# Kernel optimization log

Measured on AMD Instinct MI355X. Metric: run time of the kernel, lower is better.

## Reference

```python
import jax, jax.numpy as jnp
import numpy as np
from jax import lax

NUM_CLASSES = 10
NUM_ITER = 3
DN = ('NCHW', 'OIHW', 'NCHW')


def squash(t, axis=-1):
    sq = (t ** 2).sum(axis=axis, keepdims=True)
    return (sq / (1.0 + sq)) * t / jnp.sqrt(sq)


def setup_inputs() -> dict:
    key = jax.random.key(0)
    ks = jax.random.split(key, 12)
    B = 512
    s = 0.05  # param scale for numerical stability
    return {
        'x': jax.random.normal(ks[0], (B, 1, 28, 28), jnp.float32),
        'conv1_w': jax.random.normal(ks[1], (256, 1, 9, 9), jnp.float32) * s,
        'conv1_b': jax.random.normal(ks[2], (256,), jnp.float32) * s,
        'prim_w': jax.random.normal(ks[3], (8, 32, 256, 9, 9), jnp.float32) * s,
        'prim_b': jax.random.normal(ks[4], (8, 32), jnp.float32) * s,
        'route_w': jax.random.normal(ks[5], (NUM_CLASSES, 32 * 6 * 6, 8, 16), jnp.float32),
        'dec_w1': jax.random.normal(ks[6], (512, 16 * NUM_CLASSES), jnp.float32) * s,
        'dec_b1': jax.random.normal(ks[7], (512,), jnp.float32) * s,
        'dec_w2': jax.random.normal(ks[8], (1024, 512), jnp.float32) * s,
        'dec_b2': jax.random.normal(ks[9], (1024,), jnp.float32) * s,
        'dec_w3': jax.random.normal(ks[10], (784, 1024), jnp.float32) * s,
        'dec_b3': jax.random.normal(ks[11], (784,), jnp.float32) * s,
    }


def reference(x, conv1_w, conv1_b, prim_w, prim_b, route_w,
              dec_w1, dec_b1, dec_w2, dec_b2, dec_w3, dec_b3):
    B = x.shape[0]
    # conv1 + relu: [B,256,20,20]
    h = lax.conv_general_dilated(x, conv1_w, (1, 1), 'VALID', dimension_numbers=DN)
    h = jax.nn.relu(h + conv1_b[None, :, None, None])
    # primary capsules: 8 parallel convs fused into one conv with 8*32 out channels
    kw = prim_w.reshape(8 * 32, 256, 9, 9)
    u = lax.conv_general_dilated(h, kw, (2, 2), 'VALID', dimension_numbers=DN)
    u = u + prim_b.reshape(-1)[None, :, None, None]          # [B,256,6,6]
    u = u.reshape(B, 8, 32 * 6 * 6).transpose(0, 2, 1)       # [B,1152,8]
    u = squash(u, axis=-1)
    # digit capsules: priors [C,B,R,16]
    priors = jnp.einsum('bri,crio->cbro', u, route_w)
    logits = jnp.zeros_like(priors)
    for i in range(NUM_ITER):
        probs = jax.nn.softmax(logits, axis=2)
        v = squash((probs * priors).sum(axis=2, keepdims=True))  # [C,B,1,16]
        if i != NUM_ITER - 1:
            logits = logits + (priors * v).sum(axis=-1, keepdims=True)
    caps = v.squeeze(2).transpose(1, 0, 2)                    # [B,C,16]
    classes = jnp.sqrt((caps ** 2).sum(axis=-1))              # [B,C]
    classes = jax.nn.softmax(classes, axis=1)
    y = jax.nn.one_hot(jnp.argmax(classes, axis=1), NUM_CLASSES, dtype=caps.dtype)
    d = (caps * y[:, :, None]).reshape(B, -1)                 # [B,160]
    d = jax.nn.relu(d @ dec_w1.T + dec_b1)
    d = jax.nn.relu(d @ dec_w2.T + dec_b2)
    recon = jax.nn.sigmoid(d @ dec_w3.T + dec_b3)             # [B,784]
    return classes, recon
```

## Files before the change

### kernel.cpp

```cpp
#include <hip/hip_runtime.h>
#include <math.h>


typedef _Float16 f16;
typedef _Float16 f16x8 __attribute__((ext_vector_type(8)));
typedef _Float16 f16x4 __attribute__((ext_vector_type(4)));
typedef float f32x4 __attribute__((ext_vector_type(4)));

__device__ __forceinline__ void gl_lds16(const void* g, void* l) {
  __builtin_amdgcn_global_load_lds(
      (const __attribute__((address_space(1))) void*)g,
      (__attribute__((address_space(3))) void*)l, 16, 0, 0);
}

__global__ __launch_bounds__(256, 2) void conv1_kernel(
    const float* __restrict__ x, const float* __restrict__ w,
    const float* __restrict__ bias, f16* __restrict__ ht)
{
  __shared__ float xs[364];
  const int b = blockIdx.x;
  const int y0 = blockIdx.y * 5;
  const int t = threadIdx.x;
  for (int i = t; i < 364; i += 256) xs[i] = x[b * 784 + y0 * 28 + i];
  float wr[81];
#pragma unroll
  for (int k = 0; k < 81; ++k) wr[k] = w[t * 81 + k];
  const float bv = bias[t];
  __syncthreads();
  for (int oy = y0; oy < y0 + 5; ++oy) {
    float acc[20];
#pragma unroll
    for (int i = 0; i < 20; ++i) acc[i] = bv;
#pragma unroll
    for (int ky = 0; ky < 9; ++ky) {
      float xr[28];
#pragma unroll
      for (int q = 0; q < 7; ++q) {
        const float4 v = *(const float4*)&xs[(oy - y0 + ky) * 28 + q * 4];
        xr[q*4+0] = v.x; xr[q*4+1] = v.y; xr[q*4+2] = v.z; xr[q*4+3] = v.w;
      }
#pragma unroll
      for (int kx = 0; kx < 9; ++kx) {
        const float wv = wr[ky * 9 + kx];
#pragma unroll
        for (int ox = 0; ox < 20; ++ox) acc[ox] = fmaf(xr[ox + kx], wv, acc[ox]);
      }
    }
    f16* hp = &ht[(size_t)((b * 20 + oy) * 20) * 256 + t];
#pragma unroll
    for (int ox = 0; ox < 20; ++ox)
      hp[ox * 256] = (f16)fmaxf(acc[ox], 0.f);
  }
}

__global__ __launch_bounds__(256) void wtrans_kernel(
    const float* __restrict__ w, f16* __restrict__ wt)
{
  __shared__ float tile[64 * 83];
  const int oc = blockIdx.x;
  const int icq = blockIdx.y;
  const int t = threadIdx.x;
  const float* src = w + (size_t)oc * 20736 + (size_t)icq * 64 * 81;
  for (int idx = t; idx < 5184; idx += 256) {
    const int ici = idx / 81, kk = idx - ici * 81;
    tile[ici * 83 + kk] = src[idx];
  }
  __syncthreads();
  f16* dst = wt + (size_t)oc * 20736 + icq * 64;
  for (int idx = t; idx < 5184; idx += 256) {
    const int kk = idx >> 6, ici = idx & 63;
    dst[kk * 256 + ici] = (f16)tile[ici * 83 + kk];
  }
}

__global__ __launch_bounds__(256) void prim_mfma_kernel(
    const f16* __restrict__ ht, const f16* __restrict__ wt,
    float* __restrict__ part)
{
  __shared__ f16 sm[16384];
  const int t = threadIdx.x;
  const int wv = t >> 6, lane = t & 63;
  const int id = blockIdx.x;
  const int g = id >> 3;
  const int ks = g & 3;
  const int nb = (g >> 2) & 1;
  const int mb = (id & 7) + 8 * (g >> 3);
  const int m0 = mb * 128, n0 = nb * 128;

  const int chunk = (lane & 3) ^ ((lane >> 3) & 3);
  long aoff[2], boff[2];
#pragma unroll
  for (int i = 0; i < 2; ++i) {
    const int r = wv * 32 + i * 16 + (lane >> 2);
    const int m = m0 + r;
    const int b = m / 36, pos = m - b * 36;
    const int oy = pos / 6, ox = pos - oy * 6;
    aoff[i] = (long)(((b * 20 + 2 * oy) * 20 + 2 * ox) * 256) * 2 + chunk * 16;
    boff[i] = (long)(n0 + r) * 41472 + chunk * 16;
  }
  const char* htc = (const char*)ht;
  const char* wtc = (const char*)wt;

  const int lrow = lane & 15, quad = lane >> 4;
  const int qx = quad ^ ((lrow >> 1) & 3);
  const int wm = wv & 1, wn = wv >> 1;
  f32x4 acc[4][4] = {};

  const int s0 = ks * 162, s1 = s0 + 162;

#define STAGE(S, BUFB)                                                        \
  {                                                                           \
    const int kykx = (S) >> 3, icb = (S) & 7;                                 \
    const int ky = kykx / 9, kx = kykx - ky * 9;                              \
    const long astep = (long)((((ky * 20 + kx) * 256) + icb * 32) * 2);       \
    const long bstep = (long)(((kykx * 256) + icb * 32) * 2);                 \
    char* dA = (char*)sm + (BUFB) + wv * 2048;                                \
    char* dB = (char*)sm + (BUFB) + 8192 + wv * 2048;                         \
    gl_lds16(htc + aoff[0] + astep, dA);                                      \
    gl_lds16(htc + aoff[1] + astep, dA + 1024);                               \
    gl_lds16(wtc + boff[0] + bstep, dB);                                      \
    gl_lds16(wtc + boff[1] + bstep, dB + 1024);                               \
  }

#define CONSUME(BUFI)                                                         \
  {                                                                           \
    const f16* As = sm + (BUFI);                                              \
    const f16* Bs = sm + (BUFI) + 4096;                                       \
    f16x8 af[4], bf[4];                                                       \
    _Pragma("unroll") for (int mt = 0; mt < 4; ++mt)                          \
        af[mt] = *(const f16x8*)&As[(wm * 64 + mt * 16 + lrow) * 32 + qx * 8];\
    _Pragma("unroll") for (int nt = 0; nt < 4; ++nt)                          \
        bf[nt] = *(const f16x8*)&Bs[(wn * 64 + nt * 16 + lrow) * 32 + qx * 8];\
    _Pragma("unroll") for (int mt = 0; mt < 4; ++mt)                          \
        _Pragma("unroll") for (int nt = 0; nt < 4; ++nt)                      \
            acc[mt][nt] = __builtin_amdgcn_mfma_f32_16x16x32_f16(             \
                af[mt], bf[nt], acc[mt][nt], 0, 0, 0);                        \
  }

  STAGE(s0, 0);
  for (int s = s0; s < s1; s += 2) {
    __syncthreads();
    STAGE(s + 1, 16384);
    CONSUME(0);
    __syncthreads();
    if (s + 2 < s1) STAGE(s + 2, 0);
    CONSUME(8192);
  }
#undef STAGE
#undef CONSUME

  float* pp = part + (size_t)ks * 4718592;
#pragma unroll
  for (int mt = 0; mt < 4; ++mt) {
    const int mbase = m0 + wm * 64 + mt * 16 + quad * 4;
#pragma unroll
    for (int nt = 0; nt < 4; ++nt) {
      const int n = n0 + wn * 64 + nt * 16 + lrow;
      const int np = (n & 31) * 8 + (n >> 5);
#pragma unroll
      for (int rg = 0; rg < 4; ++rg)
        pp[(size_t)(mbase + rg) * 256 + np] = acc[mt][nt][rg];
    }
  }
}

__global__ void squash_kernel(const float* __restrict__ part,
                              const float* __restrict__ bias,
                              float* __restrict__ u)
{
  const int tid = blockIdx.x * 256 + threadIdx.x;
  if (tid >= 512 * 36 * 32) return;
  const int cc = tid & 31;
  const int row = tid >> 5;
  const int b = row / 36;
  const int pos = row - b * 36;
  const float* p = part + (size_t)row * 256 + cc * 8;
  float v[8] = {};
#pragma unroll
  for (int ksl = 0; ksl < 4; ++ksl) {
    const float4 a0 = *(const float4*)(p + (size_t)ksl * 4718592);
    const float4 a1 = *(const float4*)(p + (size_t)ksl * 4718592 + 4);
    v[0] += a0.x; v[1] += a0.y; v[2] += a0.z; v[3] += a0.w;
    v[4] += a1.x; v[5] += a1.y; v[6] += a1.z; v[7] += a1.w;
  }
  float sq = 0.f;
#pragma unroll
  for (int i = 0; i < 8; ++i) {
    v[i] += bias[i * 32 + cc];
    sq = fmaf(v[i], v[i], sq);
  }
  const float scale = sq / ((1.f + sq) * sqrtf(sq));
  float* up = &u[(size_t)(b * 1152 + cc * 36 + pos) * 8];
#pragma unroll
  for (int i = 0; i < 8; ++i) up[i] = v[i] * scale;
}

__global__ __launch_bounds__(256, 4) void priors_kernel(
    const float* __restrict__ u, const float* __restrict__ rw,
    f16* __restrict__ P)
{
  const int t = threadIdx.x;
  const int rl = t >> 2, oq = t & 3;
  const int r = blockIdx.x * 64 + rl;
  const int b0 = blockIdx.y * 64;
  const int c = blockIdx.z;

  float4 wreg[8];
  const float* wbase = rw + (size_t)(c * 1152 + r) * 128 + oq * 4;
#pragma unroll
  for (int k = 0; k < 8; ++k)
    wreg[k] = *(const float4*)(wbase + k * 16);

  f16* pbase = P + (size_t)((c * 512 + b0) * 1152 + r) * 16 + oq * 4;
  const float* ubase = u + (size_t)(b0 * 1152 + r) * 8;

  for (int b = 0; b < 64; ++b) {
    const float4 ua = *(const float4*)(ubase + (size_t)b * 9216);
    const float4 ub = *(const float4*)(ubase + (size_t)b * 9216 + 4);
    const float uu[8] = {ua.x, ua.y, ua.z, ua.w, ub.x, ub.y, ub.z, ub.w};
    float ax = 0.f, ay = 0.f, az = 0.f, aw = 0.f;
#pragma unroll
    for (int k = 0; k < 8; ++k) {
      ax = fmaf(uu[k], wreg[k].x, ax);
      ay = fmaf(uu[k], wreg[k].y, ay);
      az = fmaf(uu[k], wreg[k].z, az);
      aw = fmaf(uu[k], wreg[k].w, aw);
    }
    f16x4 st;
    st[0] = (f16)ax; st[1] = (f16)ay; st[2] = (f16)az; st[3] = (f16)aw;
    *(f16x4*)(pbase + (size_t)b * 18432) = st;
  }
}

__device__ __forceinline__ float wave_sum(float v) {
#pragma unroll
  for (int off = 32; off > 0; off >>= 1) v += __shfl_xor(v, off);
  return v;
}
__device__ __forceinline__ float wave_max(float v) {
#pragma unroll
  for (int off = 32; off > 0; off >>= 1) v = fmaxf(v, __shfl_xor(v, off));
  return v;
}

__global__ __launch_bounds__(256, 2) void routing_kernel(
    const f16* __restrict__ Pg, float* __restrict__ caps)
{
  const int c = blockIdx.x >> 9;
  const int b = blockIdx.x & 511;
  const int t = threadIdx.x;
  const int wid = t >> 6;
  const int lane = t & 63;
  __shared__ float xred[4 * 17];

  float P[5][16];
  float lg[5];
  const int nk = (t < 128) ? 5 : 4;
#pragma unroll
  for (int k = 0; k < 5; ++k)
#pragma unroll
    for (int o = 0; o < 16; ++o) P[k][o] = 0.f;

  const f16* pbase = Pg + (size_t)((c * 512 + b) * 1152) * 16;
#pragma unroll
  for (int k = 0; k < 5; ++k) {
    if (k < nk) {
      const int r = t + (k << 8);
      const f16x8 p0 = *(const f16x8*)&pbase[(size_t)r * 16];
      const f16x8 p1 = *(const f16x8*)&pbase[(size_t)r * 16 + 8];
#pragma unroll
      for (int o = 0; o < 8; ++o) {
        P[k][o]     = (float)p0[o];
        P[k][o + 8] = (float)p1[o];
      }
    }
  }

  float v[16];
  {
    float sq = 0.f;
#pragma unroll
    for (int o = 0; o < 16; ++o) {
      float p = 0.f;
#pragma unroll
      for (int k = 0; k < 5; ++k) p += P[k][o];
      p = wave_sum(p);
      if (lane == 0) xred[wid * 17 + o] = p;
      v[o] = 0.f;
    }
    __syncthreads();
#pragma unroll
    for (int o = 0; o < 16; ++o) {
      const float s = (xred[o] + xred[17 + o] + xred[34 + o] + xred[51 + o]) *
                      (1.f / 1152.f);
      v[o] = s;
      sq = fmaf(s, s, sq);
    }
    const float scale = sq / ((1.f + sq) * sqrtf(sq));
#pragma unroll
    for (int o = 0; o < 16; ++o) v[o] *= scale;
    __syncthreads();
  }
#pragma unroll
  for (int k = 0; k < 5; ++k) {
    float a = 0.f;
#pragma unroll
    for (int o = 0; o < 16; ++o) a = fmaf(P[k][o], v[o], a);
    lg[k] = a;
  }

  for (int it = 1; it < 3; ++it) {
    float m = -1e30f;
#pragma unroll
    for (int k = 0; k < 5; ++k) if (k < nk) m = fmaxf(m, lg[k]);
    m = wave_max(m);
    if (lane == 0) xred[wid * 17 + 16] = m;
    __syncthreads();
    const float mx = fmaxf(fmaxf(xred[16], xred[17 + 16]),
                           fmaxf(xred[34 + 16], xred[51 + 16]));
    __syncthreads();
    float e[5];
#pragma unroll
    for (int k = 0; k < 5; ++k) e[k] = (k < nk) ? expf(lg[k] - mx) : 0.f;
    float pS = 0.f;
#pragma unroll
    for (int k = 0; k < 5; ++k) pS += e[k];
    pS = wave_sum(pS);
    if (lane == 0) xred[wid * 17 + 16] = pS;
#pragma unroll
    for (int o = 0; o < 16; ++o) {
      float p = 0.f;
#pragma unroll
      for (int k = 0; k < 5; ++k) p = fmaf(e[k], P[k][o], p);
      p = wave_sum(p);
      if (lane == 0) xred[wid * 17 + o] = p;
    }
    __syncthreads();
    const float S = xred[16] + xred[17 + 16] + xred[34 + 16] + xred[51 + 16];
    const float inv = 1.f / S;
    float sq = 0.f;
#pragma unroll
    for (int o = 0; o < 16; ++o) {
      const float s = (xred[o] + xred[17 + o] + xred[34 + o] + xred[51 + o]) * inv;
      v[o] = s;
      sq = fmaf(s, s, sq);
    }
    const float scale = sq / ((1.f + sq) * sqrtf(sq));
#pragma unroll
    for (int o = 0; o < 16; ++o) v[o] *= scale;
    __syncthreads();
    if (it < 2) {
#pragma unroll
      for (int k = 0; k < 5; ++k) {
        float a = 0.f;
#pragma unroll
        for (int o = 0; o < 16; ++o) a = fmaf(P[k][o], v[o], a);
        lg[k] += a;
      }
    }
  }
  if (t == 0) {
    float* cp = &caps[(b * 10 + c) * 16];
#pragma unroll
    for (int o = 0; o < 16; ++o) cp[o] = v[o];
  }
}

__global__ void classes_kernel(const float* __restrict__ caps,
                               float* __restrict__ out_classes,
                               float* __restrict__ d0)
{
  const int b = blockIdx.x * 256 + threadIdx.x;
  if (b >= 512) return;
  float nrm[10];
#pragma unroll
  for (int cc = 0; cc < 10; ++cc) {
    float sq = 0.f;
#pragma unroll
    for (int o = 0; o < 16; ++o) {
      const float vv = caps[(b * 10 + cc) * 16 + o];
      sq = fmaf(vv, vv, sq);
    }
    nrm[cc] = sqrtf(sq);
  }
  float mx = nrm[0]; int cs = 0;
#pragma unroll
  for (int cc = 1; cc < 10; ++cc)
    if (nrm[cc] > mx) { mx = nrm[cc]; cs = cc; }
  float e[10], ssum = 0.f;
#pragma unroll
  for (int cc = 0; cc < 10; ++cc) { e[cc] = expf(nrm[cc] - mx); ssum += e[cc]; }
  const float inv = 1.f / ssum;
#pragma unroll
  for (int cc = 0; cc < 10; ++cc) out_classes[b * 10 + cc] = e[cc] * inv;
#pragma unroll
  for (int cc = 0; cc < 10; ++cc)
#pragma unroll
    for (int o = 0; o < 16; ++o)
      d0[b * 160 + cc * 16 + o] = (cc == cs) ? caps[(b * 10 + cc) * 16 + o] : 0.f;
}

__global__ __launch_bounds__(256, 2) void fc_kernel(
    const float* __restrict__ A, const float* __restrict__ W,
    const float* __restrict__ bias, float* __restrict__ C,
    int N, int K, int act)
{
  __shared__ float As[64][17];
  __shared__ float Ws[64][17];
  const int t = threadIdx.x;
  const int tm = t >> 4, tn = t & 15;
  const int m0 = blockIdx.y << 6, n0 = blockIdx.x << 6;
  const int lr = t >> 2, lq = (t & 3) << 2;
  float acc[4][4] = {};
  for (int k0 = 0; k0 < K; k0 += 16) {
    const float4 av = *(const float4*)&A[(m0 + lr) * K + k0 + lq];
    float4 wv = make_float4(0.f, 0.f, 0.f, 0.f);
    const int wn = n0 + lr;
    if (wn < N) wv = *(const float4*)&W[wn * K + k0 + lq];
    __syncthreads();
    As[lr][lq+0] = av.x; As[lr][lq+1] = av.y; As[lr][lq+2] = av.z; As[lr][lq+3] = av.w;
    Ws[lr][lq+0] = wv.x; Ws[lr][lq+1] = wv.y; Ws[lr][lq+2] = wv.z; Ws[lr][lq+3] = wv.w;
    __syncthreads();
#pragma unroll
    for (int kk = 0; kk < 16; ++kk) {
      float a[4], w[4];
#pragma unroll
      for (int i = 0; i < 4; ++i) a[i] = As[tm * 4 + i][kk];
#pragma unroll
      for (int j = 0; j < 4; ++j) w[j] = Ws[tn * 4 + j][kk];
#pragma unroll
      for (int i = 0; i < 4; ++i)
#pragma unroll
        for (int j = 0; j < 4; ++j) acc[i][j] = fmaf(a[i], w[j], acc[i][j]);
    }
  }
#pragma unroll
  for (int i = 0; i < 4; ++i) {
    const int m = m0 + tm * 4 + i;
#pragma unroll
    for (int j = 0; j < 4; ++j) {
      const int n = n0 + tn * 4 + j;
      if (n < N) {
        float vv = acc[i][j] + bias[n];
        vv = act ? (1.f / (1.f + expf(-vv))) : fmaxf(vv, 0.f);
        C[m * N + n] = vv;
      }
    }
  }
}

extern "C" void kernel_launch(void* const* d_in, const int* in_sizes, int n_in,
                              void* d_out, int out_size, void* d_ws, size_t ws_size,
                              hipStream_t stream)
{
  const float* x       = (const float*)d_in[0];
  const float* conv1_w = (const float*)d_in[1];
  const float* conv1_b = (const float*)d_in[2];
  const float* prim_w  = (const float*)d_in[3];
  const float* prim_b  = (const float*)d_in[4];
  const float* route_w = (const float*)d_in[5];
  const float* dec_w1  = (const float*)d_in[6];
  const float* dec_b1  = (const float*)d_in[7];
  const float* dec_w2  = (const float*)d_in[8];
  const float* dec_b2  = (const float*)d_in[9];
  const float* dec_w3  = (const float*)d_in[10];
  const float* dec_b3  = (const float*)d_in[11];
  float* out = (float*)d_out;

  char* ws = (char*)d_ws;
  f16*   ht   = (f16*)(ws);
  f16*   wtp  = (f16*)(ws + 104857600);
  float* part = (float*)(ws + 115474432);
  float* u    = (float*)(ws + 190971904);
  f16*   P    = (f16*)(ws);
  float* caps = (float*)(ws + 209846272);
  float* d0   = (float*)(ws + 210173952);
  float* d1   = (float*)(ws + 210501632);
  float* d2   = (float*)(ws + 211550208);

  hipLaunchKernelGGL(conv1_kernel, dim3(512, 4), dim3(256), 0, stream,
                     x, conv1_w, conv1_b, ht);
  hipLaunchKernelGGL(wtrans_kernel, dim3(256, 4), dim3(256), 0, stream,
                     prim_w, wtp);
  hipLaunchKernelGGL(prim_mfma_kernel, dim3(1152), dim3(256), 0, stream,
                     ht, wtp, part);
  hipLaunchKernelGGL(squash_kernel, dim3(2304), dim3(256), 0, stream,
                     part, prim_b, u);
  hipLaunchKernelGGL(priors_kernel, dim3(18, 8, 10), dim3(256), 0, stream,
                     u, route_w, P);
  hipLaunchKernelGGL(routing_kernel, dim3(5120), dim3(256), 0, stream,
                     P, caps);
  hipLaunchKernelGGL(classes_kernel, dim3(2), dim3(256), 0, stream,
                     caps, out, d0);
  hipLaunchKernelGGL(fc_kernel, dim3(8, 8), dim3(256), 0, stream,
                     d0, dec_w1, dec_b1, d1, 512, 160, 0);
  hipLaunchKernelGGL(fc_kernel, dim3(16, 8), dim3(256), 0, stream,
                     d1, dec_w2, dec_b2, d2, 1024, 512, 0);
  hipLaunchKernelGGL(fc_kernel, dim3(13, 8), dim3(256), 0, stream,
                     d2, dec_w3, dec_b3, out + 5120, 784, 1024, 1);
}
```

Baseline: 799.7 us.

## Pre-swizzle primary-capsule weights into MFMA fragment order and load B directly to registers

The weight transpose kernel now writes prim weights in a fragment-ready layout, so each lane can load its 8-element B operand for the MFMA directly from global memory into registers. This removes B staging through LDS and halves the shared-memory footprint, with B fragments double-buffered in registers. It also reorders the squashed capsule layout (pos-major instead of channel-major), with the priors kernel remapping route weight indices to match, which should make the squash stores more contiguous. The risk is that direct global loads of B may expose more latency, and the per-wave B loads are repeated across blocks that share the same weights.

```diff
diff --git a/kernel.cpp b/kernel.cpp
--- a/kernel.cpp
+++ b/kernel.cpp
@@ -54,30 +54,31 @@
 }
 
 __global__ __launch_bounds__(256) void wtrans_kernel(
-    const float* __restrict__ w, f16* __restrict__ wt)
-{
-  __shared__ float tile[64 * 83];
+    const float* __restrict__ w, f16* __restrict__ wtf)
+{
+  __shared__ f16 ls[20736];
   const int oc = blockIdx.x;
-  const int icq = blockIdx.y;
+  const int T = oc >> 4, lrow = oc & 15;
   const int t = threadIdx.x;
-  const float* src = w + (size_t)oc * 20736 + (size_t)icq * 64 * 81;
-  for (int idx = t; idx < 5184; idx += 256) {
-    const int ici = idx / 81, kk = idx - ici * 81;
-    tile[ici * 83 + kk] = src[idx];
-  }
+  const float* src = w + (size_t)oc * 20736;
+  for (int idx = t; idx < 20736; idx += 256) ls[idx] = (f16)src[idx];
   __syncthreads();
-  f16* dst = wt + (size_t)oc * 20736 + icq * 64;
-  for (int idx = t; idx < 5184; idx += 256) {
-    const int kk = idx >> 6, ici = idx & 63;
-    dst[kk * 256 + ici] = (f16)tile[ici * 83 + kk];
+  for (int c = t; c < 2592; c += 256) {
+    const int s = c >> 2, quad = c & 3;
+    const int kykx = s >> 3, icb = s & 7;
+    f16x8 v;
+#pragma unroll
+    for (int j = 0; j < 8; ++j)
+      v[j] = ls[(icb * 32 + quad * 8 + j) * 81 + kykx];
+    *(f16x8*)&wtf[((size_t)(T * 648 + s) * 64 + quad * 16 + lrow) * 8] = v;
   }
 }
 
 __global__ __launch_bounds__(256) void prim_mfma_kernel(
-    const f16* __restrict__ ht, const f16* __restrict__ wt,
+    const f16* __restrict__ ht, const f16* __restrict__ wtf,
     float* __restrict__ part)
 {
-  __shared__ f16 sm[16384];
+  __shared__ f16 smA[8192];
   const int t = threadIdx.x;
   const int wv = t >> 6, lane = t & 63;
   const int id = blockIdx.x;
@@ -88,7 +89,7 @@
   const int m0 = mb * 128, n0 = nb * 128;
 
   const int chunk = (lane & 3) ^ ((lane >> 3) & 3);
-  long aoff[2], boff[2];
+  long aoff[2];
 #pragma unroll
   for (int i = 0; i < 2; ++i) {
     const int r = wv * 32 + i * 16 + (lane >> 2);
@@ -96,57 +97,65 @@
     const int b = m / 36, pos = m - b * 36;
     const int oy = pos / 6, ox = pos - oy * 6;
     aoff[i] = (long)(((b * 20 + 2 * oy) * 20 + 2 * ox) * 256) * 2 + chunk * 16;
-    boff[i] = (long)(n0 + r) * 41472 + chunk * 16;
   }
   const char* htc = (const char*)ht;
-  const char* wtc = (const char*)wt;
 
   const int lrow = lane & 15, quad = lane >> 4;
   const int qx = quad ^ ((lrow >> 1) & 3);
   const int wm = wv & 1, wn = wv >> 1;
+
+  const f16* bp[4];
+#pragma unroll
+  for (int nt = 0; nt < 4; ++nt)
+    bp[nt] = wtf + (size_t)(nb * 8 + wn * 4 + nt) * 648 * 512 + lane * 8;
+
   f32x4 acc[4][4] = {};
-
   const int s0 = ks * 162, s1 = s0 + 162;
 
-#define STAGE(S, BUFB)                                                        \
+#define STAGE_A(S, BUFB)                                                      \
   {                                                                           \
     const int kykx = (S) >> 3, icb = (S) & 7;                                 \
     const int ky = kykx / 9, kx = kykx - ky * 9;                              \
     const long astep = (long)((((ky * 20 + kx) * 256) + icb * 32) * 2);       \
-    const long bstep = (long)(((kykx * 256) + icb * 32) * 2);                 \
-    char* dA = (char*)sm + (BUFB) + wv * 2048;                                \
-    char* dB = (char*)sm + (BUFB) + 8192 + wv * 2048;                         \
+    char* dA = (char*)smA + (BUFB) + wv * 2048;                               \
     gl_lds16(htc + aoff[0] + astep, dA);                                      \
     gl_lds16(htc + aoff[1] + astep, dA + 1024);                               \
-    gl_lds16(wtc + boff[0] + bstep, dB);                                      \
-    gl_lds16(wtc + boff[1] + bstep, dB + 1024);                               \
-  }
-
-#define CONSUME(BUFI)                                                         \
+  }
+
+#define CONSUME(BUFI, BF)                                                     \
   {                                                                           \
-    const f16* As = sm + (BUFI);                                              \
-    const f16* Bs = sm + (BUFI) + 4096;                                       \
-    f16x8 af[4], bf[4];                                                       \
+    const f16* As = smA + (BUFI);                                             \
+    f16x8 af[4];                                                              \
     _Pragma("unroll") for (int mt = 0; mt < 4; ++mt)                          \
         af[mt] = *(const f16x8*)&As[(wm * 64 + mt * 16 + lrow) * 32 + qx * 8];\
-    _Pragma("unroll") for (int nt = 0; nt < 4; ++nt)                          \
-        bf[nt] = *(const f16x8*)&Bs[(wn * 64 + nt * 16 + lrow) * 32 + qx * 8];\
     _Pragma("unroll") for (int mt = 0; mt < 4; ++mt)                          \
         _Pragma("unroll") for (int nt = 0; nt < 4; ++nt)                      \
             acc[mt][nt] = __builtin_amdgcn_mfma_f32_16x16x32_f16(             \
-                af[mt], bf[nt], acc[mt][nt], 0, 0, 0);                        \
-  }
-
-  STAGE(s0, 0);
+                af[mt], (BF)[nt], acc[mt][nt], 0, 0, 0);                      \
+  }
+
+  f16x8 bfA[4], bfB[4];
+#pragma unroll
+  for (int nt = 0; nt < 4; ++nt)
+    bfA[nt] = *(const f16x8*)(bp[nt] + (size_t)s0 * 512);
+  STAGE_A(s0, 0);
   for (int s = s0; s < s1; s += 2) {
     __syncthreads();
-    STAGE(s + 1, 16384);
-    CONSUME(0);
-    __syncthreads();
-    if (s + 2 < s1) STAGE(s + 2, 0);
-    CONSUME(8192);
-  }
-#undef STAGE
+    STAGE_A(s + 1, 8192);
+#pragma unroll
+    for (int nt = 0; nt < 4; ++nt)
+      bfB[nt] = *(const f16x8*)(bp[nt] + (size_t)(s + 1) * 512);
+    CONSUME(0, bfA);
+    __syncthreads();
+    if (s + 2 < s1) {
+      STAGE_A(s + 2, 0);
+#pragma unroll
+      for (int nt = 0; nt < 4; ++nt)
+        bfA[nt] = *(const f16x8*)(bp[nt] + (size_t)(s + 2) * 512);
+    }
+    CONSUME(4096, bfB);
+  }
+#undef STAGE_A
 #undef CONSUME
 
   float* pp = part + (size_t)ks * 4718592;
@@ -190,7 +199,7 @@
     sq = fmaf(v[i], v[i], sq);
   }
   const float scale = sq / ((1.f + sq) * sqrtf(sq));
-  float* up = &u[(size_t)(b * 1152 + cc * 36 + pos) * 8];
+  float* up = &u[(size_t)(b * 1152 + pos * 32 + cc) * 8];
 #pragma unroll
   for (int i = 0; i < 8; ++i) up[i] = v[i] * scale;
 }
@@ -201,18 +210,20 @@
 {
   const int t = threadIdx.x;
   const int rl = t >> 2, oq = t & 3;
-  const int r = blockIdx.x * 64 + rl;
+  const int rs = blockIdx.x * 64 + rl;
+  const int pos = rs >> 5, cc = rs & 31;
+  const int r_true = cc * 36 + pos;
   const int b0 = blockIdx.y * 64;
   const int c = blockIdx.z;
 
   float4 wreg[8];
-  const float* wbase = rw + (size_t)(c * 1152 + r) * 128 + oq * 4;
+  const float* wbase = rw + (size_t)(c * 1152 + r_true) * 128 + oq * 4;
 #pragma unroll
   for (int k = 0; k < 8; ++k)
     wreg[k] = *(const float4*)(wbase + k * 16);
 
-  f16* pbase = P + (size_t)((c * 512 + b0) * 1152 + r) * 16 + oq * 4;
-  const float* ubase = u + (size_t)(b0 * 1152 + r) * 8;
+  f16* pbase = P + (size_t)((c * 512 + b0) * 1152 + rs) * 16 + oq * 4;
+  const float* ubase = u + (size_t)(b0 * 1152 + rs) * 8;
 
   for (int b = 0; b < 64; ++b) {
     const float4 ua = *(const float4*)(ubase + (size_t)b * 9216);
@@ -469,7 +480,7 @@
 
   char* ws = (char*)d_ws;
   f16*   ht   = (f16*)(ws);
-  f16*   wtp  = (f16*)(ws + 104857600);
+  f16*   wtf  = (f16*)(ws + 104857600);
   float* part = (float*)(ws + 115474432);
   float* u    = (float*)(ws + 190971904);
   f16*   P    = (f16*)(ws);
@@ -480,10 +491,10 @@
 
   hipLaunchKernelGGL(conv1_kernel, dim3(512, 4), dim3(256), 0, stream,
                      x, conv1_w, conv1_b, ht);
-  hipLaunchKernelGGL(wtrans_kernel, dim3(256, 4), dim3(256), 0, stream,
-                     prim_w, wtp);
+  hipLaunchKernelGGL(wtrans_kernel, dim3(256), dim3(256), 0, stream,
+                     prim_w, wtf);
   hipLaunchKernelGGL(prim_mfma_kernel, dim3(1152), dim3(256), 0, stream,
-                     ht, wtp, part);
+                     ht, wtf, part);
   hipLaunchKernelGGL(squash_kernel, dim3(2304), dim3(256), 0, stream,
                      part, prim_b, u);
   hipLaunchKernelGGL(priors_kernel, dim3(18, 8, 10), dim3(256), 0, stream,
```

Measured after the change: 820.4 us. +2.6%, slower.

## Run conv1 as im2col plus MFMA GEMM and store squashed capsules in fp16

Applied to the files above, without the earlier changes.

Replaces the direct FP32 conv1 with an im2col pass into a padded fp16 matrix (K=96), a transposed fp16 weight, and a 128x128-tile MFMA GEMM with fused bias and ReLU. Squash now writes fp16 capsules in a position-major order, and priors reads them with a single vector load while remapping route weights to the true capsule index. This moves conv1 FLOPs onto matrix cores and halves capsule traffic. In exchange it adds two extra kernels, the im2col buffer traffic, and fp16 rounding of the conv1 inputs and weights.

```diff
diff --git a/kernel.cpp b/kernel.cpp
--- a/kernel.cpp
+++ b/kernel.cpp
@@ -13,43 +13,102 @@
       (__attribute__((address_space(3))) void*)l, 16, 0, 0);
 }
 
-__global__ __launch_bounds__(256, 2) void conv1_kernel(
-    const float* __restrict__ x, const float* __restrict__ w,
+__global__ void im2col_kernel(const float* __restrict__ x, f16* __restrict__ A)
+{
+  const int c = blockIdx.x * 256 + threadIdx.x;
+  const int m = c / 12, kc = c - m * 12;
+  const int b = m / 400, rem = m - b * 400;
+  const int oy = rem / 20, ox = rem - oy * 20;
+  const float* xb = x + b * 784;
+  f16x8 v;
+#pragma unroll
+  for (int j = 0; j < 8; ++j) {
+    const int k = kc * 8 + j;
+    float val = 0.f;
+    if (k < 81) {
+      const int ky = k / 9, kx = k - ky * 9;
+      val = xb[(oy + ky) * 28 + ox + kx];
+    }
+    v[j] = (f16)val;
+  }
+  *(f16x8*)&A[(size_t)m * 96 + kc * 8] = v;
+}
+
+__global__ void c1trans_kernel(const float* __restrict__ w, f16* __restrict__ wt1)
+{
+  const int idx = blockIdx.x * 256 + threadIdx.x;
+  const int oc = idx / 96, k = idx - oc * 96;
+  wt1[idx] = (k < 81) ? (f16)w[oc * 81 + k] : (f16)0.f;
+}
+
+__global__ __launch_bounds__(256) void conv1_mfma_kernel(
+    const f16* __restrict__ A, const f16* __restrict__ wt1,
     const float* __restrict__ bias, f16* __restrict__ ht)
 {
-  __shared__ float xs[364];
-  const int b = blockIdx.x;
-  const int y0 = blockIdx.y * 5;
+  __shared__ f16 sm[8192];
   const int t = threadIdx.x;
-  for (int i = t; i < 364; i += 256) xs[i] = x[b * 784 + y0 * 28 + i];
-  float wr[81];
-#pragma unroll
-  for (int k = 0; k < 81; ++k) wr[k] = w[t * 81 + k];
-  const float bv = bias[t];
-  __syncthreads();
-  for (int oy = y0; oy < y0 + 5; ++oy) {
-    float acc[20];
-#pragma unroll
-    for (int i = 0; i < 20; ++i) acc[i] = bv;
-#pragma unroll
-    for (int ky = 0; ky < 9; ++ky) {
-      float xr[28];
-#pragma unroll
-      for (int q = 0; q < 7; ++q) {
-        const float4 v = *(const float4*)&xs[(oy - y0 + ky) * 28 + q * 4];
-        xr[q*4+0] = v.x; xr[q*4+1] = v.y; xr[q*4+2] = v.z; xr[q*4+3] = v.w;
-      }
-#pragma unroll
-      for (int kx = 0; kx < 9; ++kx) {
-        const float wv = wr[ky * 9 + kx];
-#pragma unroll
-        for (int ox = 0; ox < 20; ++ox) acc[ox] = fmaf(xr[ox + kx], wv, acc[ox]);
-      }
-    }
-    f16* hp = &ht[(size_t)((b * 20 + oy) * 20) * 256 + t];
-#pragma unroll
-    for (int ox = 0; ox < 20; ++ox)
-      hp[ox * 256] = (f16)fmaxf(acc[ox], 0.f);
+  const int wv = t >> 6, lane = t & 63;
+  const int id = blockIdx.x;
+  const int mb = id >> 1, nb = id & 1;
+  const int m0 = mb * 128, n0 = nb * 128;
+
+  const int chunk = (lane & 3) ^ ((lane >> 3) & 3);
+  long aoff[2], boff[2];
+#pragma unroll
+  for (int i = 0; i < 2; ++i) {
+    const int r = wv * 32 + i * 16 + (lane >> 2);
+    aoff[i] = (long)(m0 + r) * 192 + chunk * 16;
+    boff[i] = (long)(n0 + r) * 192 + chunk * 16;
+  }
+  const char* ac = (const char*)A;
+  const char* bc = (const char*)wt1;
+
+  const int lrow = lane & 15, quad = lane >> 4;
+  const int qx = quad ^ ((lrow >> 1) & 3);
+  const int wm = wv & 1, wn = wv >> 1;
+  f32x4 acc[4][4] = {};
+
+  for (int s = 0; s < 3; ++s) {
+    const long kstep = (long)s * 64;
+    __syncthreads();
+    {
+      char* dA = (char*)sm + wv * 2048;
+      char* dB = (char*)sm + 8192 + wv * 2048;
+      gl_lds16(ac + aoff[0] + kstep, dA);
+      gl_lds16(ac + aoff[1] + kstep, dA + 1024);
+      gl_lds16(bc + boff[0] + kstep, dB);
+      gl_lds16(bc + boff[1] + kstep, dB + 1024);
+    }
+    __syncthreads();
+    const f16* As = sm;
+    const f16* Bs = sm + 4096;
+    f16x8 af[4], bf[4];
+#pragma unroll
+    for (int mt = 0; mt < 4; ++mt)
+      af[mt] = *(const f16x8*)&As[(wm * 64 + mt * 16 + lrow) * 32 + qx * 8];
+#pragma unroll
+    for (int nt = 0; nt < 4; ++nt)
+      bf[nt] = *(const f16x8*)&Bs[(wn * 64 + nt * 16 + lrow) * 32 + qx * 8];
+#pragma unroll
+    for (int mt = 0; mt < 4; ++mt)
+#pragma unroll
+      for (int nt = 0; nt < 4; ++nt)
+        acc[mt][nt] = __builtin_amdgcn_mfma_f32_16x16x32_f16(
+            af[mt], bf[nt], acc[mt][nt], 0, 0, 0);
+  }
+
+#pragma unroll
+  for (int nt = 0; nt < 4; ++nt) {
+    const int n = n0 + wn * 64 + nt * 16 + lrow;
+    const float bv = bias[n];
+#pragma unroll
+    for (int mt = 0; mt < 4; ++mt) {
+      const int mbase = m0 + wm * 64 + mt * 16 + quad * 4;
+#pragma unroll
+      for (int rg = 0; rg < 4; ++rg)
+        ht[(size_t)(mbase + rg) * 256 + n] =
+            (f16)fmaxf(acc[mt][nt][rg] + bv, 0.f);
+    }
   }
 }
 
@@ -166,7 +225,7 @@
 
 __global__ void squash_kernel(const float* __restrict__ part,
                               const float* __restrict__ bias,
-                              float* __restrict__ u)
+                              f16* __restrict__ u16)
 {
   const int tid = blockIdx.x * 256 + threadIdx.x;
   if (tid >= 512 * 36 * 32) return;
@@ -190,41 +249,43 @@
     sq = fmaf(v[i], v[i], sq);
   }
   const float scale = sq / ((1.f + sq) * sqrtf(sq));
-  float* up = &u[(size_t)(b * 1152 + cc * 36 + pos) * 8];
-#pragma unroll
-  for (int i = 0; i < 8; ++i) up[i] = v[i] * scale;
+  f16x8 st;
+#pragma unroll
+  for (int i = 0; i < 8; ++i) st[i] = (f16)(v[i] * scale);
+  *(f16x8*)&u16[(size_t)(b * 1152 + pos * 32 + cc) * 8] = st;
 }
 
 __global__ __launch_bounds__(256, 4) void priors_kernel(
-    const float* __restrict__ u, const float* __restrict__ rw,
+    const f16* __restrict__ u16, const float* __restrict__ rw,
     f16* __restrict__ P)
 {
   const int t = threadIdx.x;
   const int rl = t >> 2, oq = t & 3;
-  const int r = blockIdx.x * 64 + rl;
+  const int rs = blockIdx.x * 64 + rl;
+  const int pos = rs >> 5, cc = rs & 31;
+  const int r_true = cc * 36 + pos;
   const int b0 = blockIdx.y * 64;
   const int c = blockIdx.z;
 
   float4 wreg[8];
-  const float* wbase = rw + (size_t)(c * 1152 + r) * 128 + oq * 4;
+  const float* wbase = rw + (size_t)(c * 1152 + r_true) * 128 + oq * 4;
 #pragma unroll
   for (int k = 0; k < 8; ++k)
     wreg[k] = *(const float4*)(wbase + k * 16);
 
-  f16* pbase = P + (size_t)((c * 512 + b0) * 1152 + r) * 16 + oq * 4;
-  const float* ubase = u + (size_t)(b0 * 1152 + r) * 8;
+  f16* pbase = P + (size_t)((c * 512 + b0) * 1152 + rs) * 16 + oq * 4;
+  const f16* ubase = u16 + (size_t)(b0 * 1152 + rs) * 8;
 
   for (int b = 0; b < 64; ++b) {
-    const float4 ua = *(const float4*)(ubase + (size_t)b * 9216);
-    const float4 ub = *(const float4*)(ubase + (size_t)b * 9216 + 4);
-    const float uu[8] = {ua.x, ua.y, ua.z, ua.w, ub.x, ub.y, ub.z, ub.w};
+    const f16x8 uv = *(const f16x8*)(ubase + (size_t)b * 9216);
     float ax = 0.f, ay = 0.f, az = 0.f, aw = 0.f;
 #pragma unroll
     for (int k = 0; k < 8; ++k) {
-      ax = fmaf(uu[k], wreg[k].x, ax);
-      ay = fmaf(uu[k], wreg[k].y, ay);
-      az = fmaf(uu[k], wreg[k].z, az);
-      aw = fmaf(uu[k], wreg[k].w, aw);
+      const float uk = (float)uv[k];
+      ax = fmaf(uk, wreg[k].x, ax);
+      ay = fmaf(uk, wreg[k].y, ay);
+      az = fmaf(uk, wreg[k].z, az);
+      aw = fmaf(uk, wreg[k].w, aw);
     }
     f16x4 st;
     st[0] = (f16)ax; st[1] = (f16)ay; st[2] = (f16)az; st[3] = (f16)aw;
@@ -471,23 +532,28 @@
   f16*   ht   = (f16*)(ws);
   f16*   wtp  = (f16*)(ws + 104857600);
   float* part = (float*)(ws + 115474432);
-  float* u    = (float*)(ws + 190971904);
+  f16*   A16  = (f16*)(ws + 115474432);
+  f16*   wt1  = (f16*)(ws + 190971904);
+  f16*   u16  = (f16*)(ws + 191021056);
   f16*   P    = (f16*)(ws);
-  float* caps = (float*)(ws + 209846272);
-  float* d0   = (float*)(ws + 210173952);
-  float* d1   = (float*)(ws + 210501632);
-  float* d2   = (float*)(ws + 211550208);
-
-  hipLaunchKernelGGL(conv1_kernel, dim3(512, 4), dim3(256), 0, stream,
-                     x, conv1_w, conv1_b, ht);
+  float* caps = (float*)(ws + 200458240);
+  float* d0   = (float*)(ws + 200785920);
+  float* d1   = (float*)(ws + 201113600);
+  float* d2   = (float*)(ws + 202162176);
+
+  hipLaunchKernelGGL(im2col_kernel, dim3(9600), dim3(256), 0, stream, x, A16);
+  hipLaunchKernelGGL(c1trans_kernel, dim3(96), dim3(256), 0, stream,
+                     conv1_w, wt1);
+  hipLaunchKernelGGL(conv1_mfma_kernel, dim3(3200), dim3(256), 0, stream,
+                     A16, wt1, conv1_b, ht);
   hipLaunchKernelGGL(wtrans_kernel, dim3(256, 4), dim3(256), 0, stream,
                      prim_w, wtp);
   hipLaunchKernelGGL(prim_mfma_kernel, dim3(1152), dim3(256), 0, stream,
                      ht, wtp, part);
   hipLaunchKernelGGL(squash_kernel, dim3(2304), dim3(256), 0, stream,
-                     part, prim_b, u);
+                     part, prim_b, u16);
   hipLaunchKernelGGL(priors_kernel, dim3(18, 8, 10), dim3(256), 0, stream,
-                     u, route_w, P);
+                     u16, route_w, P);
   hipLaunchKernelGGL(routing_kernel, dim3(5120), dim3(256), 0, stream,
                      P, caps);
   hipLaunchKernelGGL(classes_kernel, dim3(2), dim3(256), 0, stream,
```

After: 762.5 us. 1.05x faster.
